# Kernel tuning notes

Measured on AMD Instinct MI355X. Metric: run time of the kernel, lower is better.

## Reference

```python
import jax, jax.numpy as jnp
import numpy as np

N = 100000      # nodes
E = 1200000     # edges
D_IN = 128      # input_dim
H = 64          # hidden_dim
OUT = 3         # output_dim
EPS = 1e-5      # BatchNorm eps


def setup_inputs() -> dict:
    key = jax.random.key(0)
    ks = jax.random.split(key, 24)
    w = lambda k, shape: jax.random.normal(k, shape, jnp.float32) * 0.05
    return {
        "x": jax.random.normal(ks[0], (N, D_IN), jnp.float32),
        "edge_index": jax.random.randint(ks[1], (2, E), 0, N, dtype=jnp.int32),
        "proj_W": w(ks[2], (H, D_IN)), "proj_b": w(ks[3], (H,)),
        "conv1_W": w(ks[4], (H, H)), "conv1_b": w(ks[5], (H,)),
        "bn1_g": jnp.ones((H,), jnp.float32), "bn1_b": w(ks[6], (H,)),
        "conv2_W": w(ks[7], (H, H)), "conv2_b": w(ks[8], (H,)),
        "bn2_g": jnp.ones((H,), jnp.float32), "bn2_b": w(ks[9], (H,)),
        "conv3_W": w(ks[10], (H, H)), "conv3_b": w(ks[11], (H,)),
        "bn3_g": jnp.ones((H,), jnp.float32), "bn3_b": w(ks[12], (H,)),
        "byp_W": w(ks[13], (OUT, D_IN)), "byp_b": w(ks[14], (OUT,)),
        "head_W": w(ks[15], (OUT, H + OUT)), "head_b": w(ks[16], (OUT,)),
    }


def reference(x, edge_index, proj_W, proj_b,
              conv1_W, conv1_b, bn1_g, bn1_b,
              conv2_W, conv2_b, bn2_g, bn2_b,
              conv3_W, conv3_b, bn3_g, bn3_b,
              byp_W, byp_b, head_W, head_b):
    n = x.shape[0]
    row, col = edge_index[0], edge_index[1]
    loop = jnp.arange(n, dtype=row.dtype)
    row_f = jnp.concatenate([row, loop])   # source (with self loops)
    col_f = jnp.concatenate([col, loop])   # target
    # symmetric GCN normalization: deg over targets of A+I, edge weight 1
    deg = jax.ops.segment_sum(jnp.ones(row_f.shape, jnp.float32), col_f, num_segments=n)
    dinv = jnp.where(deg > 0, jax.lax.rsqrt(deg), 0.0)
    norm = dinv[row_f] * dinv[col_f]       # [E+N]

    def gcn(h, W, b):
        h = h @ W.T                                    # transform then propagate
        msg = h[row_f] * norm[:, None]                 # gather + scale
        return jax.ops.segment_sum(msg, col_f, num_segments=n) + b

    def bn(h, g, b):
        # eval-mode BatchNorm1d: running_mean=0, running_var=1 buffers
        return h * (g / jnp.sqrt(1.0 + EPS)) + b

    h = x @ proj_W.T + proj_b
    idn = h
    h = jax.nn.relu(bn(gcn(h, conv1_W, conv1_b), bn1_g, bn1_b)) + idn  # dropout inactive (eval)
    idn = h
    h = jax.nn.relu(bn(gcn(h, conv2_W, conv2_b), bn2_g, bn2_b)) + idn
    h = jax.nn.relu(bn(gcn(h, conv3_W, conv3_b), bn3_g, bn3_b))

    byp = x @ byp_W.T + byp_b
    p = jnp.concatenate([h, byp], axis=1) @ head_W.T + head_b
    kappa = jnp.clip(p[:, 0] * 5.0 + 2.5, 0.2, 10.0)
    alpha = p[:, 1]
    tau = jnp.clip(p[:, 2] + 0.5, 0.05, 2.0)
    return jnp.stack([kappa, alpha, tau], axis=1)
```

## Files before the change

### kernel.cpp

```cpp
#include <hip/hip_runtime.h>
#include <hip/hip_fp16.h>

#define NN 100000
#define NE 1200000
#define NBUK ((NN + 127) / 128)
#define NCHUNK 128

typedef _Float16 h8 __attribute__((ext_vector_type(8)));
typedef float f32x4 __attribute__((ext_vector_type(4)));

__global__ __launch_bounds__(1024) void k_zerob(int* bcnt) {
    int i = threadIdx.x;
    if (i <= NBUK) bcnt[i] = 0;
}

__global__ __launch_bounds__(256) void k_bhist(const int* __restrict__ col, int* __restrict__ bcnt) {
    __shared__ int lh[NBUK];
    for (int i = threadIdx.x; i < NBUK; i += 256) lh[i] = 0;
    __syncthreads();
    for (int e = blockIdx.x * 256 + threadIdx.x; e < NE; e += 256 * 256)
        atomicAdd(&lh[col[e] >> 7], 1);
    __syncthreads();
    for (int i = threadIdx.x; i < NBUK; i += 256) {
        int v = lh[i];
        if (v) atomicAdd(&bcnt[i], v);
    }
}

__global__ __launch_bounds__(1024) void k_bscan(int* __restrict__ bcnt, int* __restrict__ bcur) {
    __shared__ int s[1024];
    int tid = threadIdx.x;
    int v = (tid < NBUK) ? bcnt[tid] : 0;
    s[tid] = v;
    __syncthreads();
    #pragma unroll
    for (int d = 1; d < 1024; d <<= 1) {
        int t = (tid >= d) ? s[tid - d] : 0;
        __syncthreads();
        s[tid] += t;
        __syncthreads();
    }
    if (tid < NBUK) {
        int excl = s[tid] - v;
        bcnt[tid] = excl;
        bcur[tid] = excl;
    }
    if (tid == 0) bcnt[NBUK] = NE;
}

__global__ __launch_bounds__(256) void k_bucket(const int* __restrict__ row,
                                                const int* __restrict__ col,
                                                int* __restrict__ bcur,
                                                unsigned* __restrict__ tmp) {
    __shared__ int lh[NBUK];
    const int tid = threadIdx.x;
    const int per = (NE + NCHUNK - 1) / NCHUNK;
    const int e0 = blockIdx.x * per;
    const int e1 = (e0 + per < NE) ? (e0 + per) : NE;
    for (int i = tid; i < NBUK; i += 256) lh[i] = 0;
    __syncthreads();
    for (int e = e0 + tid; e < e1; e += 256)
        atomicAdd(&lh[col[e] >> 7], 1);
    __syncthreads();
    for (int b = tid; b < NBUK; b += 256) {
        int c = lh[b];
        if (c) lh[b] = atomicAdd(&bcur[b], c);
    }
    __syncthreads();
    for (int e = e0 + tid; e < e1; e += 256) {
        int c = col[e], r = row[e];
        int pos = atomicAdd(&lh[c >> 7], 1);
        tmp[pos] = ((unsigned)r << 7) | (unsigned)(c & 127);
    }
}

__global__ __launch_bounds__(256) void k_build(const unsigned* __restrict__ tmp,
                                               const int* __restrict__ bbase,
                                               int* __restrict__ off,
                                               float* __restrict__ dinv,
                                               int* __restrict__ csr_row) {
    __shared__ int cnt[128], s[128], cur[128];
    const int b = blockIdx.x, tid = threadIdx.x;
    const int colBase = b << 7;
    const int nCols = (NN - colBase < 128) ? (NN - colBase) : 128;
    const int seg0 = bbase[b], seg1 = bbase[b + 1];
    if (tid < 128) cnt[tid] = 0;
    __syncthreads();
    for (int i = seg0 + tid; i < seg1; i += 256)
        atomicAdd(&cnt[tmp[i] & 127], 1);
    __syncthreads();
    if (tid < 128) s[tid] = cnt[tid];
    __syncthreads();
    #pragma unroll
    for (int d = 1; d < 128; d <<= 1) {
        int t = (tid < 128 && tid >= d) ? s[tid - d] : 0;
        __syncthreads();
        if (tid < 128) s[tid] += t;
        __syncthreads();
    }
    if (tid < nCols) {
        int exc = seg0 + s[tid] - cnt[tid];
        off[colBase + tid] = exc;
        cur[tid] = exc;
        dinv[colBase + tid] = rsqrtf((float)cnt[tid] + 1.0f);
    }
    if (b == 0 && tid == 0) off[NN] = NE;
    __syncthreads();
    for (int i = seg0 + tid; i < seg1; i += 256) {
        unsigned v = tmp[i];
        int pos = atomicAdd(&cur[v & 127u], 1);
        csr_row[pos] = (int)(v >> 7);
    }
}

__global__ __launch_bounds__(256) void k_gemmP(const float* __restrict__ X,
                                               const float* __restrict__ W,
                                               const float* __restrict__ bias,
                                               _Float16* __restrict__ Yh,
                                               const float* __restrict__ bypW,
                                               const float* __restrict__ bypb,
                                               float* __restrict__ bypOut,
                                               int n_nodes) {
    constexpr int D = 128, RS = D + 8, KS = D / 32;
    __shared__ _Float16 Xh[64 * RS];
    __shared__ _Float16 Wh[64 * RS];
    const int tid = threadIdx.x;
    const int n0 = blockIdx.x * 64;

    for (int i = tid; i < 64 * (D / 8); i += 256) {
        int j = i / (D / 8), d8 = (i % (D / 8)) * 8;
        const float4* wp = (const float4*)&W[j * D + d8];
        float4 w0 = wp[0], w1 = wp[1];
        h8 h = { (_Float16)w0.x, (_Float16)w0.y, (_Float16)w0.z, (_Float16)w0.w,
                 (_Float16)w1.x, (_Float16)w1.y, (_Float16)w1.z, (_Float16)w1.w };
        *(h8*)&Wh[j * RS + d8] = h;
    }
    for (int i = tid; i < 64 * (D / 8); i += 256) {
        int nl = i / (D / 8), d8 = (i % (D / 8)) * 8;
        int n = n0 + nl; if (n >= n_nodes) n = n_nodes - 1;
        const float4* xp = (const float4*)&X[(size_t)n * D + d8];
        float4 x0 = xp[0], x1 = xp[1];
        h8 h = { (_Float16)x0.x, (_Float16)x0.y, (_Float16)x0.z, (_Float16)x0.w,
                 (_Float16)x1.x, (_Float16)x1.y, (_Float16)x1.z, (_Float16)x1.w };
        *(h8*)&Xh[nl * RS + d8] = h;
    }
    __syncthreads();

    const int wid = tid >> 6, lane = tid & 63;
    const int lm = lane & 15, lq = lane >> 4;
    const int mBase = wid * 16;

    h8 bfrag[4][KS];
    #pragma unroll
    for (int t = 0; t < 4; ++t)
        #pragma unroll
        for (int s = 0; s < KS; ++s)
            bfrag[t][s] = *(const h8*)&Wh[(t * 16 + lm) * RS + s * 32 + lq * 8];

    h8 bfragB[KS];
    #pragma unroll
    for (int s = 0; s < KS; ++s) {
        if (lm < 3) {
            const float4* wp = (const float4*)&bypW[lm * D + s * 32 + lq * 8];
            float4 w0 = wp[0], w1 = wp[1];
            bfragB[s] = (h8){ (_Float16)w0.x, (_Float16)w0.y, (_Float16)w0.z, (_Float16)w0.w,
                              (_Float16)w1.x, (_Float16)w1.y, (_Float16)w1.z, (_Float16)w1.w };
        } else {
            bfragB[s] = (h8)(_Float16)0;
        }
    }

    f32x4 acc[5] = {};
    #pragma unroll
    for (int s = 0; s < KS; ++s) {
        h8 a = *(const h8*)&Xh[(mBase + lm) * RS + s * 32 + lq * 8];
        #pragma unroll
        for (int t = 0; t < 4; ++t)
            acc[t] = __builtin_amdgcn_mfma_f32_16x16x32_f16(a, bfrag[t][s], acc[t], 0, 0, 0);
        acc[4] = __builtin_amdgcn_mfma_f32_16x16x32_f16(a, bfragB[s], acc[4], 0, 0, 0);
    }

    float bb[4];
    #pragma unroll
    for (int t = 0; t < 4; ++t) bb[t] = bias[t * 16 + lm];
    float bypbv = (lm < 3) ? bypb[lm] : 0.f;
    const int nodeBase = n0 + mBase + lq * 4;
    #pragma unroll
    for (int r = 0; r < 4; ++r) {
        int node = nodeBase + r;
        if (node < n_nodes) {
            #pragma unroll
            for (int t = 0; t < 4; ++t)
                Yh[(size_t)node * 64 + t * 16 + lm] = (_Float16)(acc[t][r] + bb[t]);
            if (lm < 3)
                bypOut[node * 3 + lm] = acc[4][r] + bypbv;
        }
    }
}

__global__ __launch_bounds__(256) void k_gemmC(const _Float16* __restrict__ Xhg,
                                               const float* __restrict__ W,
                                               const float* __restrict__ dinv,
                                               _Float16* __restrict__ Yh,
                                               int n_nodes) {
    constexpr int D = 64, RS = D + 8, KS = D / 32;
    __shared__ _Float16 Xh[64 * RS];
    __shared__ _Float16 Wh[64 * RS];
    const int tid = threadIdx.x;
    const int n0 = blockIdx.x * 64;

    for (int i = tid; i < 64 * (D / 8); i += 256) {
        int j = i / (D / 8), d8 = (i % (D / 8)) * 8;
        const float4* wp = (const float4*)&W[j * D + d8];
        float4 w0 = wp[0], w1 = wp[1];
        h8 h = { (_Float16)w0.x, (_Float16)w0.y, (_Float16)w0.z, (_Float16)w0.w,
                 (_Float16)w1.x, (_Float16)w1.y, (_Float16)w1.z, (_Float16)w1.w };
        *(h8*)&Wh[j * RS + d8] = h;
    }
    for (int i = tid; i < 64 * (D / 8); i += 256) {
        int nl = i / (D / 8), d8 = (i % (D / 8)) * 8;
        int n = n0 + nl; if (n >= n_nodes) n = n_nodes - 1;
        *(h8*)&Xh[nl * RS + d8] = *(const h8*)&Xhg[(size_t)n * D + d8];
    }
    __syncthreads();

    const int wid = tid >> 6, lane = tid & 63;
    const int lm = lane & 15, lq = lane >> 4;
    const int mBase = wid * 16;

    h8 bfrag[4][KS];
    #pragma unroll
    for (int t = 0; t < 4; ++t)
        #pragma unroll
        for (int s = 0; s < KS; ++s)
            bfrag[t][s] = *(const h8*)&Wh[(t * 16 + lm) * RS + s * 32 + lq * 8];

    f32x4 acc[4] = {};
    #pragma unroll
    for (int s = 0; s < KS; ++s) {
        h8 a = *(const h8*)&Xh[(mBase + lm) * RS + s * 32 + lq * 8];
        #pragma unroll
        for (int t = 0; t < 4; ++t)
            acc[t] = __builtin_amdgcn_mfma_f32_16x16x32_f16(a, bfrag[t][s], acc[t], 0, 0, 0);
    }

    const int nodeBase = n0 + mBase + lq * 4;
    #pragma unroll
    for (int r = 0; r < 4; ++r) {
        int node = nodeBase + r;
        if (node < n_nodes) {
            float sdv = dinv[node];
            #pragma unroll
            for (int t = 0; t < 4; ++t)
                Yh[(size_t)node * 64 + t * 16 + lm] = (_Float16)(acc[t][r] * sdv);
        }
    }
}

template<bool RES, bool HEAD>
__global__ __launch_bounds__(256) void k_gather(const _Float16* __restrict__ hBh,
                                                const float* __restrict__ dinv,
                                                const int* __restrict__ off,
                                                const int* __restrict__ csr_row,
                                                const float* __restrict__ convb,
                                                const float* __restrict__ bng,
                                                const float* __restrict__ bnb,
                                                _Float16* __restrict__ hA,
                                                const float* __restrict__ byp,
                                                const float* __restrict__ headW,
                                                const float* __restrict__ headb,
                                                float* __restrict__ out) {
    __shared__ float HWs[HEAD ? 204 : 1];
    const int tid = threadIdx.x;
    if constexpr (HEAD) {
        for (int i = tid; i < 204; i += 256)
            HWs[i] = (i < 201) ? headW[i] : headb[i - 201];
        __syncthreads();
    }
    const int wid = tid >> 6, lane = tid & 63;
    const int n = blockIdx.x * 32 + wid * 8 + (lane >> 3);
    const int oct = lane & 7;
    const int f0 = oct * 8;

    const int e0 = off[n], eEnd = off[n + 1];
    const int deg = eEnd - e0;
    int m = deg;
    #pragma unroll
    for (int mask = 8; mask < 64; mask <<= 1) {
        int o = __shfl_xor(m, mask, 64);
        m = (o > m) ? o : m;
    }

    h8 acch = *(const h8*)(hBh + ((size_t)n << 6) + f0);
    const h8 zero = (h8)(_Float16)0;
    for (int it = 0; it < m; it += 4) {
        bool v0 = it < deg, v1 = it + 1 < deg, v2 = it + 2 < deg, v3 = it + 3 < deg;
        int i0 = e0 + it;
        int r0 = csr_row[v0 ? i0 : 0];
        int r1 = csr_row[v1 ? i0 + 1 : 0];
        int r2 = csr_row[v2 ? i0 + 2 : 0];
        int r3 = csr_row[v3 ? i0 + 3 : 0];
        h8 raw0 = *(const h8*)(hBh + ((size_t)r0 << 6) + f0);
        h8 raw1 = *(const h8*)(hBh + ((size_t)r1 << 6) + f0);
        h8 raw2 = *(const h8*)(hBh + ((size_t)r2 << 6) + f0);
        h8 raw3 = *(const h8*)(hBh + ((size_t)r3 << 6) + f0);
        acch = acch + (v0 ? raw0 : zero);
        acch = acch + (v1 ? raw1 : zero);
        acch = acch + (v2 ? raw2 : zero);
        acch = acch + (v3 ? raw3 : zero);
    }

    const float dv = dinv[n];
    const float bnscale = rsqrtf(1.0f + 1e-5f);
    const float4 cb0 = *(const float4*)&convb[f0], cb1 = *(const float4*)&convb[f0 + 4];
    const float4 g0  = *(const float4*)&bng[f0],  g1  = *(const float4*)&bng[f0 + 4];
    const float4 b0_ = *(const float4*)&bnb[f0],  b1_ = *(const float4*)&bnb[f0 + 4];
    const float cb[8] = { cb0.x, cb0.y, cb0.z, cb0.w, cb1.x, cb1.y, cb1.z, cb1.w };
    const float gg[8] = { g0.x, g0.y, g0.z, g0.w, g1.x, g1.y, g1.z, g1.w };
    const float bb[8] = { b0_.x, b0_.y, b0_.z, b0_.w, b1_.x, b1_.y, b1_.z, b1_.w };
    float v[8];
    #pragma unroll
    for (int j = 0; j < 8; ++j)
        v[j] = fmaxf(((float)acch[j] * dv + cb[j]) * (gg[j] * bnscale) + bb[j], 0.0f);

    if constexpr (!HEAD) {
        size_t o = ((size_t)n << 6) + f0;
        if constexpr (RES) {
            h8 old = *(const h8*)&hA[o];
            #pragma unroll
            for (int j = 0; j < 8; ++j) v[j] += (float)old[j];
        }
        h8 res = { (_Float16)v[0], (_Float16)v[1], (_Float16)v[2], (_Float16)v[3],
                   (_Float16)v[4], (_Float16)v[5], (_Float16)v[6], (_Float16)v[7] };
        *(h8*)&hA[o] = res;
    } else {
        float p[3];
        #pragma unroll
        for (int o = 0; o < 3; ++o) {
            float t = 0.f;
            #pragma unroll
            for (int j = 0; j < 8; ++j) t += v[j] * HWs[o * 67 + f0 + j];
            p[o] = t;
        }
        #pragma unroll
        for (int mask = 1; mask < 8; mask <<= 1) {
            #pragma unroll
            for (int o = 0; o < 3; ++o) p[o] += __shfl_xor(p[o], mask, 64);
        }
        if (oct == 0) {
            float by0 = byp[n * 3], by1 = byp[n * 3 + 1], by2 = byp[n * 3 + 2];
            #pragma unroll
            for (int o = 0; o < 3; ++o)
                p[o] += by0 * HWs[o * 67 + 64] + by1 * HWs[o * 67 + 65] + by2 * HWs[o * 67 + 66]
                      + HWs[201 + o];
            float kappa = fminf(fmaxf(p[0] * 5.0f + 2.5f, 0.2f), 10.0f);
            float tau   = fminf(fmaxf(p[2] + 0.5f, 0.05f), 2.0f);
            out[(size_t)n * 3]     = kappa;
            out[(size_t)n * 3 + 1] = p[1];
            out[(size_t)n * 3 + 2] = tau;
        }
    }
}

extern "C" void kernel_launch(void* const* d_in, const int* in_sizes, int n_in,
                              void* d_out, int out_size, void* d_ws, size_t ws_size,
                              hipStream_t stream) {
    const float* x     = (const float*)d_in[0];
    const int*   ei    = (const int*)d_in[1];
    const int*   row   = ei;
    const int*   col   = ei + NE;
    const float* projW = (const float*)d_in[2];
    const float* projb = (const float*)d_in[3];
    const float* convW[3] = { (const float*)d_in[4], (const float*)d_in[8],  (const float*)d_in[12] };
    const float* convb[3] = { (const float*)d_in[5], (const float*)d_in[9],  (const float*)d_in[13] };
    const float* bng[3]   = { (const float*)d_in[6], (const float*)d_in[10], (const float*)d_in[14] };
    const float* bnb[3]   = { (const float*)d_in[7], (const float*)d_in[11], (const float*)d_in[15] };
    const float* bypW  = (const float*)d_in[16];
    const float* bypb  = (const float*)d_in[17];
    const float* headW = (const float*)d_in[18];
    const float* headb = (const float*)d_in[19];
    float* out = (float*)d_out;

    float*    ws   = (float*)d_ws;
    float*    dinv = ws;
    _Float16* hAh  = (_Float16*)(ws + 102400);
    _Float16* hBh  = hAh + (size_t)NN * 64;
    float*    byp  = (float*)(hBh + (size_t)NN * 64);
    int*      off     = (int*)(byp + 300032);
    int*      csr_row = off + 100096;
    int*      bcnt    = csr_row + NE;
    int*      bcur    = bcnt + 784;
    unsigned* tmp     = (unsigned*)hAh;

    k_zerob<<<1, 1024, 0, stream>>>(bcnt);
    k_bhist<<<256, 256, 0, stream>>>(col, bcnt);
    k_bscan<<<1, 1024, 0, stream>>>(bcnt, bcur);
    k_bucket<<<NCHUNK, 256, 0, stream>>>(row, col, bcur, tmp);
    k_build<<<NBUK, 256, 0, stream>>>(tmp, bcnt, off, dinv, csr_row);

    k_gemmP<<<(NN + 63) / 64, 256, 0, stream>>>(x, projW, projb, hAh, bypW, bypb, byp, NN);

    for (int l = 0; l < 3; l++) {
        k_gemmC<<<(NN + 63) / 64, 256, 0, stream>>>(hAh, convW[l], dinv, hBh, NN);
        if (l < 2)
            k_gather<true, false><<<NN / 32, 256, 0, stream>>>(
                hBh, dinv, off, csr_row, convb[l], bng[l], bnb[l], hAh,
                nullptr, nullptr, nullptr, nullptr);
        else
            k_gather<false, true><<<NN / 32, 256, 0, stream>>>(
                hBh, dinv, off, csr_row, convb[l], bng[l], bnb[l], nullptr,
                byp, headW, headb, out);
    }
}
```

Baseline: 285.9 us.

## Replace atomic bucket offsets with per-block count matrix and column scan

The bucketing phase now records each chunk's per-bucket histogram in a matrix and uses a per-bucket scan across chunks to derive deterministic offsets. This replaces the separate global histogram kernel, the zeroing kernel and the global atomics on bucket cursors. The column is read one fewer time and the global atomic contention is gone, but an extra scan kernel launch is added and the workspace must hold the NBUK x NCHUNK count matrix.

```diff
diff --git a/kernel.cpp b/kernel.cpp
--- a/kernel.cpp
+++ b/kernel.cpp
@@ -9,49 +9,8 @@
 typedef _Float16 h8 __attribute__((ext_vector_type(8)));
 typedef float f32x4 __attribute__((ext_vector_type(4)));
 
-__global__ __launch_bounds__(1024) void k_zerob(int* bcnt) {
-    int i = threadIdx.x;
-    if (i <= NBUK) bcnt[i] = 0;
-}
-
-__global__ __launch_bounds__(256) void k_bhist(const int* __restrict__ col, int* __restrict__ bcnt) {
-    __shared__ int lh[NBUK];
-    for (int i = threadIdx.x; i < NBUK; i += 256) lh[i] = 0;
-    __syncthreads();
-    for (int e = blockIdx.x * 256 + threadIdx.x; e < NE; e += 256 * 256)
-        atomicAdd(&lh[col[e] >> 7], 1);
-    __syncthreads();
-    for (int i = threadIdx.x; i < NBUK; i += 256) {
-        int v = lh[i];
-        if (v) atomicAdd(&bcnt[i], v);
-    }
-}
-
-__global__ __launch_bounds__(1024) void k_bscan(int* __restrict__ bcnt, int* __restrict__ bcur) {
-    __shared__ int s[1024];
-    int tid = threadIdx.x;
-    int v = (tid < NBUK) ? bcnt[tid] : 0;
-    s[tid] = v;
-    __syncthreads();
-    #pragma unroll
-    for (int d = 1; d < 1024; d <<= 1) {
-        int t = (tid >= d) ? s[tid - d] : 0;
-        __syncthreads();
-        s[tid] += t;
-        __syncthreads();
-    }
-    if (tid < NBUK) {
-        int excl = s[tid] - v;
-        bcnt[tid] = excl;
-        bcur[tid] = excl;
-    }
-    if (tid == 0) bcnt[NBUK] = NE;
-}
-
-__global__ __launch_bounds__(256) void k_bucket(const int* __restrict__ row,
-                                                const int* __restrict__ col,
-                                                int* __restrict__ bcur,
-                                                unsigned* __restrict__ tmp) {
+__global__ __launch_bounds__(256) void k_bucketA(const int* __restrict__ col,
+                                                 int* __restrict__ blkcnt) {
     __shared__ int lh[NBUK];
     const int tid = threadIdx.x;
     const int per = (NE + NCHUNK - 1) / NCHUNK;
@@ -62,10 +21,56 @@
     for (int e = e0 + tid; e < e1; e += 256)
         atomicAdd(&lh[col[e] >> 7], 1);
     __syncthreads();
-    for (int b = tid; b < NBUK; b += 256) {
-        int c = lh[b];
-        if (c) lh[b] = atomicAdd(&bcur[b], c);
-    }
+    for (int b = tid; b < NBUK; b += 256)
+        blkcnt[b * NCHUNK + blockIdx.x] = lh[b];
+}
+
+__global__ __launch_bounds__(128) void k_colscan(int* __restrict__ blkcnt, int* __restrict__ bcnt) {
+    __shared__ int s[NCHUNK];
+    const int b = blockIdx.x, tid = threadIdx.x;
+    int v = blkcnt[b * NCHUNK + tid];
+    s[tid] = v;
+    __syncthreads();
+    #pragma unroll
+    for (int d = 1; d < NCHUNK; d <<= 1) {
+        int t = (tid >= d) ? s[tid - d] : 0;
+        __syncthreads();
+        s[tid] += t;
+        __syncthreads();
+    }
+    blkcnt[b * NCHUNK + tid] = s[tid] - v;
+    if (tid == NCHUNK - 1) bcnt[b] = s[NCHUNK - 1];
+}
+
+__global__ __launch_bounds__(1024) void k_bscan(int* __restrict__ bcnt) {
+    __shared__ int s[1024];
+    int tid = threadIdx.x;
+    int v = (tid < NBUK) ? bcnt[tid] : 0;
+    s[tid] = v;
+    __syncthreads();
+    #pragma unroll
+    for (int d = 1; d < 1024; d <<= 1) {
+        int t = (tid >= d) ? s[tid - d] : 0;
+        __syncthreads();
+        s[tid] += t;
+        __syncthreads();
+    }
+    if (tid < NBUK) bcnt[tid] = s[tid] - v;
+    if (tid == 0) bcnt[NBUK] = NE;
+}
+
+__global__ __launch_bounds__(256) void k_bucketB(const int* __restrict__ row,
+                                                 const int* __restrict__ col,
+                                                 const int* __restrict__ bbase,
+                                                 const int* __restrict__ blkcnt,
+                                                 unsigned* __restrict__ tmp) {
+    __shared__ int lh[NBUK];
+    const int tid = threadIdx.x;
+    const int per = (NE + NCHUNK - 1) / NCHUNK;
+    const int e0 = blockIdx.x * per;
+    const int e1 = (e0 + per < NE) ? (e0 + per) : NE;
+    for (int b = tid; b < NBUK; b += 256)
+        lh[b] = bbase[b] + blkcnt[b * NCHUNK + blockIdx.x];
     __syncthreads();
     for (int e = e0 + tid; e < e1; e += 256) {
         int c = col[e], r = row[e];
@@ -389,13 +394,13 @@
     int*      off     = (int*)(byp + 300032);
     int*      csr_row = off + 100096;
     int*      bcnt    = csr_row + NE;
-    int*      bcur    = bcnt + 784;
+    int*      blkcnt  = bcnt + 784;
     unsigned* tmp     = (unsigned*)hAh;
 
-    k_zerob<<<1, 1024, 0, stream>>>(bcnt);
-    k_bhist<<<256, 256, 0, stream>>>(col, bcnt);
-    k_bscan<<<1, 1024, 0, stream>>>(bcnt, bcur);
-    k_bucket<<<NCHUNK, 256, 0, stream>>>(row, col, bcur, tmp);
+    k_bucketA<<<NCHUNK, 256, 0, stream>>>(col, blkcnt);
+    k_colscan<<<NBUK, 128, 0, stream>>>(blkcnt, bcnt);
+    k_bscan<<<1, 1024, 0, stream>>>(bcnt);
+    k_bucketB<<<NCHUNK, 256, 0, stream>>>(row, col, bcnt, blkcnt, tmp);
     k_build<<<NBUK, 256, 0, stream>>>(tmp, bcnt, off, dinv, csr_row);
 
     k_gemmP<<<(NN + 63) / 64, 256, 0, stream>>>(x, projW, projb, hAh, bypW, bypb, byp, NN);
```

Measured after the change: 281.5 us. About the same (-1.5%).
